# Optimization experiments

Measured on AMD Instinct MI355X. Metric: run time of the kernel, lower is better.

Reference implementation:

```python
import jax, jax.numpy as jnp
import numpy as np

B, K, S, HS = 32, 8, 512, 256


def setup_inputs() -> dict:
    key = jax.random.key(0)
    ks = jax.random.split(key, 12)
    sc = 1.0 / np.sqrt(HS)
    return {
        "rem_fea": jax.random.normal(ks[0], (B, S, HS), jnp.float32),
        "ret_fea": jax.random.normal(ks[1], (B, K, S, HS), jnp.float32),
        "Wr": jax.random.normal(ks[2], (HS, HS), jnp.float32) * sc,
        "br": jax.random.normal(ks[3], (HS,), jnp.float32) * sc,
        "Wt": jax.random.normal(ks[4], (HS, HS), jnp.float32) * sc,
        "bt": jax.random.normal(ks[5], (HS,), jnp.float32) * sc,
        "W1": jax.random.normal(ks[6], (K, HS, HS), jnp.float32) * sc,
        "b1": jax.random.normal(ks[7], (K, HS), jnp.float32) * sc,
        "W2": jax.random.normal(ks[8], (K, HS, HS), jnp.float32) * sc,
        "b2": jax.random.normal(ks[9], (K, HS), jnp.float32) * sc,
    }


def reference(rem_fea, ret_fea, Wr, br, Wt, bt, W1, b1, W2, b2):
    # ---- MACRouter ----
    rem_lin = rem_fea @ Wr + br                       # [B,S,hs]
    ret_lin = jnp.einsum("bksd,de->bkse", ret_fea, Wt) + bt  # [B,K,S,hs]
    avg_rem = rem_lin.mean(axis=1)                    # [B,hs]
    avg_ret = ret_lin.mean(axis=2)                    # [B,K,hs]
    scores = jnp.einsum("bd,bkd->bk", avg_rem, avg_ret)
    routing = jax.nn.softmax(scores, axis=1)          # [B,K]
    # ---- K dense experts (batched over K) ----
    h = jax.nn.relu(jnp.einsum("bksd,kde->bkse", ret_fea, W1) + b1[None, :, None, :])
    expert_outs = jnp.einsum("bksd,kde->bkse", h, W2) + b2[None, :, None, :]
    # ---- weighted sum over experts ----
    gen_fea = jnp.einsum("bksd,bk->bsd", expert_outs, routing)
    return gen_fea
```

## Files before the change

### kernel.cpp

```cpp
#include <hip/hip_runtime.h>
#include <hip/hip_bf16.h>

typedef __attribute__((ext_vector_type(8))) short bf16x8;
typedef __attribute__((ext_vector_type(4))) float f32x4;

constexpr int Bb = 32, Kk = 8, Ss = 512, HS = 256;
constexpr int SUB = 32;
constexpr int NST = Ss / SUB;
constexpr int SUB_BYTES = SUB * HS * 2;
constexpr int MT = 64;

__device__ __forceinline__ unsigned short f2bf(float f) {
  unsigned int u = __builtin_bit_cast(unsigned int, f);
  u = (u + 0x7FFFu + ((u >> 16) & 1u)) >> 16;
  return (unsigned short)u;
}

__device__ __forceinline__ void gload_lds16(const void* g, void* l) {
  __builtin_amdgcn_global_load_lds((const __attribute__((address_space(1))) void*)g,
                                   (__attribute__((address_space(3))) void*)l, 16, 0, 0);
}

__global__ void prep(const float* __restrict__ rem, const float* __restrict__ ret,
                     const float* __restrict__ W1, const float* __restrict__ W2,
                     unsigned short* __restrict__ W1p, unsigned short* __restrict__ W2p,
                     char* __restrict__ swz, float* __restrict__ partial_ret,
                     float* __restrict__ partial_rem) {
  int blk = blockIdx.x, t = threadIdx.x;
  if (blk < 512) {
    const float* W = (blk < 256) ? W1 : W2;
    unsigned short* Wp = (blk < 256) ? W1p : W2p;
    int idx = (blk & 255) * 256 + t;
    int lane = idx & 63, nt = (idx >> 6) & 15, kk = (idx >> 10) & 7, k = idx >> 13;
    const float* src = W + ((size_t)k * HS + kk * 32 + ((lane >> 4) * 8)) * HS + nt * 16 + (lane & 15);
    unsigned short* dst = Wp + (size_t)idx * 8;
#pragma unroll
    for (int i = 0; i < 8; ++i) dst[i] = f2bf(src[(size_t)i * HS]);
    return;
  }
  blk -= 512;
  const float* src;
  float* pdst;
  char* dst = nullptr;
  if (blk < Bb * Kk * NST) {
    int st = blk & 15, bk = blk >> 4;
    src = ret + ((size_t)bk * Ss + st * SUB) * HS;
    pdst = partial_ret + (size_t)blk * HS;
    if (swz) dst = swz + (size_t)blk * SUB_BYTES;
  } else {
    int rid = blk - Bb * Kk * NST;
    int st = rid & 15, b = rid >> 4;
    src = rem + ((size_t)b * Ss + st * SUB) * HS;
    pdst = partial_rem + (size_t)rid * HS;
  }
  f32x4 acc = {0.f, 0.f, 0.f, 0.f};
#pragma unroll
  for (int j = 0; j < 8; ++j) {
    int f = j * 256 + t;
    int row = f >> 6, c4 = f & 63;
    f32x4 v = *reinterpret_cast<const f32x4*>(src + (size_t)row * HS + c4 * 4);
    acc += v;
    if (dst) {
      union { unsigned short h[4]; unsigned long long u; } pk;
      pk.h[0] = f2bf(v[0]); pk.h[1] = f2bf(v[1]); pk.h[2] = f2bf(v[2]); pk.h[3] = f2bf(v[3]);
      int off = (c4 >> 5) * 8192 + row * 256 + ((((c4 & 31) >> 1) ^ (row & 7)) * 16) + (c4 & 1) * 8;
      *reinterpret_cast<unsigned long long*>(dst + off) = pk.u;
    }
  }
  __shared__ f32x4 red[256];
  red[t] = acc;
  __syncthreads();
  if (t < 64) {
    f32x4 s = red[t] + red[t + 64] + red[t + 128] + red[t + 192];
    *reinterpret_cast<f32x4*>(pdst + t * 4) = s;
  }
}

template <int SRC>
__launch_bounds__(512, 1)
__global__ void experts_kernel(const float* __restrict__ ret, const char* __restrict__ ret_swz,
                               const unsigned short* __restrict__ W1p,
                               const unsigned short* __restrict__ W2p,
                               const float* __restrict__ b1, const float* __restrict__ b2,
                               const float* __restrict__ partial_ret,
                               const float* __restrict__ partial_rem,
                               const float* __restrict__ Wr, const float* __restrict__ br,
                               const float* __restrict__ Wt, const float* __restrict__ bt,
                               float* __restrict__ out) {
  __shared__ __align__(16) char A_lds[2][2 * SUB_BYTES];
  __shared__ __align__(16) char H_lds[MT * HS * 2];
  __shared__ float srem_sh[HS];
  __shared__ float sret_sh[Kk][HS];
  __shared__ float shred[8];
  __shared__ float scores_sh[Kk];
  __shared__ float routing_sh[Kk];

  const int blk = blockIdx.x;
  const int b = blk >> 3, st64 = blk & 7;
  const int tid = threadIdx.x;
  const int wave = tid >> 6, lane = tid & 63;
  const int l15 = lane & 15, l4 = lane >> 4;
  const int t256 = tid & 255, half = tid >> 8;

  auto stage = [&](int k, int bufi) {
    if constexpr (SRC == 0) {
      const char* tb = ret_swz + ((size_t)((b * Kk + k) * NST + st64 * 2)) * SUB_BYTES;
#pragma unroll
      for (int i = 0; i < 4; ++i) {
        int c = wave + i * 8;
        gload_lds16(tb + c * 1024 + (size_t)lane * 16, A_lds[bufi] + c * 1024);
      }
    } else {
      const float* src = ret + ((size_t)(b * Kk + k) * Ss + st64 * MT) * HS;
#pragma unroll
      for (int j = 0; j < 8; ++j) {
        int f = j * 512 + tid;
        int row = f >> 6, c4 = f & 63;
        f32x4 v = *reinterpret_cast<const f32x4*>(src + (size_t)row * HS + c4 * 4);
        union { unsigned short h[4]; unsigned long long u; } pk;
        pk.h[0] = f2bf(v[0]); pk.h[1] = f2bf(v[1]); pk.h[2] = f2bf(v[2]); pk.h[3] = f2bf(v[3]);
        int off = (row >> 5) * 16384 + (c4 >> 5) * 8192 + (row & 31) * 256 +
                  ((((c4 & 31) >> 1) ^ (row & 7)) * 16) + (c4 & 1) * 8;
        *reinterpret_cast<unsigned long long*>(A_lds[bufi] + off) = pk.u;
      }
    }
  };

  stage(0, 0);

  {
#pragma unroll
    for (int kk = 0; kk < 4; ++kk) {
      int k = half * 4 + kk;
      float sk = 0.f;
      for (int st = 0; st < NST; ++st)
        sk += partial_ret[((size_t)((b * Kk + k) * NST + st)) * HS + t256];
      sret_sh[k][t256] = sk;
    }
    if (half == 1) {
      float s_ = 0.f;
      for (int st = 0; st < NST; ++st)
        s_ += partial_rem[((size_t)(b * NST + st)) * HS + t256];
      srem_sh[t256] = s_;
    }
    __syncthreads();

    float rl = 0.f;
    float tl[4] = {0.f, 0.f, 0.f, 0.f};
    for (int e = 0; e < HS; ++e) {
      float wr = Wr[(size_t)e * HS + t256];
      float wt = Wt[(size_t)e * HS + t256];
      rl += srem_sh[e] * wr;
#pragma unroll
      for (int kk = 0; kk < 4; ++kk) tl[kk] += sret_sh[half * 4 + kk][e] * wt;
    }
    rl = rl * (1.f / Ss) + br[t256];

    for (int kk = 0; kk < 4; ++kk) {
      float p = rl * (tl[kk] * (1.f / Ss) + bt[t256]);
#pragma unroll
      for (int off = 32; off; off >>= 1) p += __shfl_down(p, off);
      if (lane == 0) shred[wave] = p;
      __syncthreads();
      if (tid == 0) scores_sh[kk] = shred[0] + shred[1] + shred[2] + shred[3];
      else if (tid == 256) scores_sh[4 + kk] = shred[4] + shred[5] + shred[6] + shred[7];
      __syncthreads();
    }
    if (tid == 0) {
      float mx = scores_sh[0];
      for (int k = 1; k < Kk; ++k) mx = fmaxf(mx, scores_sh[k]);
      float ssum = 0.f, ev[Kk];
      for (int k = 0; k < Kk; ++k) { ev[k] = expf(scores_sh[k] - mx); ssum += ev[k]; }
      for (int k = 0; k < Kk; ++k) routing_sh[k] = ev[k] / ssum;
    }
  }
  asm volatile("s_waitcnt vmcnt(0) lgkmcnt(0)\n\ts_barrier" ::: "memory");

  f32x4 out_acc[4][2];
#pragma unroll
  for (int m = 0; m < 4; ++m)
#pragma unroll
    for (int n = 0; n < 2; ++n) out_acc[m][n] = {0.f, 0.f, 0.f, 0.f};
  const f32x4 zero4 = {0.f, 0.f, 0.f, 0.f};

  int buf = 0;
  for (int k = 0; k < Kk; ++k) {
    const unsigned short* W1k = W1p + (size_t)k * 65536;
    bf16x8 w1f[8][2];
#pragma unroll
    for (int kk = 0; kk < 8; ++kk)
#pragma unroll
      for (int m = 0; m < 2; ++m)
        w1f[kk][m] = *reinterpret_cast<const bf16x8*>(
            W1k + ((size_t)(kk * 16 + wave * 2 + m) * 64 + lane) * 8);

    if (k + 1 < Kk) stage(k + 1, buf ^ 1);

    f32x4 accH[2][4];
#pragma unroll
    for (int m = 0; m < 2; ++m)
#pragma unroll
      for (int n = 0; n < 4; ++n) accH[m][n] = zero4;

#pragma unroll
    for (int kk = 0; kk < 8; ++kk) {
      bf16x8 aA[4];
#pragma unroll
      for (int n = 0; n < 4; ++n) {
        int srow = n * 16 + l15;
        int r5 = srow & 31;
        int off = (srow >> 5) * 16384 + (kk >> 2) * 8192 + r5 * 256 +
                  ((((kk & 3) * 4 + l4) ^ (r5 & 7)) * 16);
        aA[n] = *reinterpret_cast<const bf16x8*>(A_lds[buf] + off);
      }
#pragma unroll
      for (int m = 0; m < 2; ++m)
#pragma unroll
        for (int n = 0; n < 4; ++n)
          accH[m][n] = __builtin_amdgcn_mfma_f32_16x16x32_bf16(w1f[kk][m], aA[n], accH[m][n], 0, 0, 0);
    }

    const unsigned short* W2k = W2p + (size_t)k * 65536;
    bf16x8 w2f[8][2];
#pragma unroll
    for (int kk = 0; kk < 8; ++kk)
#pragma unroll
      for (int n = 0; n < 2; ++n)
        w2f[kk][n] = *reinterpret_cast<const bf16x8*>(
            W2k + ((size_t)(kk * 16 + wave * 2 + n) * 64 + lane) * 8);

    {
      float r = routing_sh[k];
#pragma unroll
      for (int m = 0; m < 2; ++m) {
        int e0 = wave * 32 + m * 16 + l4 * 4;
        float4 b1v = *reinterpret_cast<const float4*>(b1 + k * HS + e0);
#pragma unroll
        for (int n = 0; n < 4; ++n) {
          int srow = n * 16 + l15;
          union { unsigned short h[4]; unsigned long long u; } pk;
          pk.h[0] = f2bf(fmaxf(accH[m][n][0] + b1v.x, 0.f) * r);
          pk.h[1] = f2bf(fmaxf(accH[m][n][1] + b1v.y, 0.f) * r);
          pk.h[2] = f2bf(fmaxf(accH[m][n][2] + b1v.z, 0.f) * r);
          pk.h[3] = f2bf(fmaxf(accH[m][n][3] + b1v.w, 0.f) * r);
          int boff = srow * 512 + ((e0 * 2) ^ ((srow & 7) << 4));
          *reinterpret_cast<unsigned long long*>(H_lds + boff) = pk.u;
        }
      }
    }

    asm volatile("s_waitcnt lgkmcnt(0)\n\ts_barrier" ::: "memory");

#pragma unroll
    for (int kk = 0; kk < 8; ++kk) {
      bf16x8 aH[4];
#pragma unroll
      for (int m = 0; m < 4; ++m) {
        int r = m * 16 + l15;
        int boff = r * 512 + ((kk * 64 + l4 * 16) ^ ((r & 7) << 4));
        aH[m] = *reinterpret_cast<const bf16x8*>(H_lds + boff);
      }
#pragma unroll
      for (int m = 0; m < 4; ++m)
#pragma unroll
        for (int n = 0; n < 2; ++n)
          out_acc[m][n] = __builtin_amdgcn_mfma_f32_16x16x32_bf16(aH[m], w2f[kk][n], out_acc[m][n], 0, 0, 0);
    }
    asm volatile("s_waitcnt vmcnt(0) lgkmcnt(0)\n\ts_barrier" ::: "memory");
    buf ^= 1;
  }

  float bias2[2];
#pragma unroll
  for (int n = 0; n < 2; ++n) {
    int col = (wave * 2 + n) * 16 + l15;
    float s = 0.f;
#pragma unroll
    for (int k = 0; k < Kk; ++k) s += routing_sh[k] * b2[k * HS + col];
    bias2[n] = s;
  }
#pragma unroll
  for (int m = 0; m < 4; ++m)
#pragma unroll
    for (int i = 0; i < 4; ++i) {
      int row = m * 16 + l4 * 4 + i;
      float* orow = out + ((size_t)b * Ss + st64 * MT + row) * HS;
#pragma unroll
      for (int n = 0; n < 2; ++n)
        orow[(wave * 2 + n) * 16 + l15] = out_acc[m][n][i] + bias2[n];
    }
}

extern "C" void kernel_launch(void* const* d_in, const int* in_sizes, int n_in,
                              void* d_out, int out_size, void* d_ws, size_t ws_size,
                              hipStream_t stream) {
  const float* rem = (const float*)d_in[0];
  const float* ret = (const float*)d_in[1];
  const float* Wr  = (const float*)d_in[2];
  const float* br  = (const float*)d_in[3];
  const float* Wt  = (const float*)d_in[4];
  const float* bt  = (const float*)d_in[5];
  const float* W1  = (const float*)d_in[6];
  const float* b1  = (const float*)d_in[7];
  const float* W2  = (const float*)d_in[8];
  const float* b2  = (const float*)d_in[9];
  float* out = (float*)d_out;

  char* w = (char*)d_ws;
  unsigned short* W1p = (unsigned short*)w;
  unsigned short* W2p = (unsigned short*)(w + (1u << 20));
  float* partial_ret  = (float*)(w + (2u << 20));
  float* partial_rem  = (float*)(w + (6u << 20));
  char*  ret_swz      = w + (7u << 20);

  bool full = ws_size >= ((size_t)71 << 20);

  prep<<<512 + Bb * Kk * NST + Bb * NST, 256, 0, stream>>>(rem, ret, W1, W2, W1p, W2p,
                                                           full ? ret_swz : nullptr,
                                                           partial_ret, partial_rem);
  if (full)
    experts_kernel<0><<<Bb * (Ss / MT), 512, 0, stream>>>(ret, ret_swz, W1p, W2p, b1, b2,
                                                          partial_ret, partial_rem,
                                                          Wr, br, Wt, bt, out);
  else
    experts_kernel<1><<<Bb * (Ss / MT), 512, 0, stream>>>(ret, nullptr, W1p, W2p, b1, b2,
                                                          partial_ret, partial_rem,
                                                          Wr, br, Wt, bt, out);
}
```

Baseline: 99.21 us.

## Drop pre-swizzled bf16 ret copy; register-prefetch fp32 tiles into LDS

Removes the prep-stage write of a swizzled bf16 copy of ret_fea and the experts kernel's direct global-to-LDS loads from it. The experts kernel now loads fp32 ret tiles into registers one expert ahead, then converts and writes them into the swizzled LDS buffer after the first GEMM's barrier. This avoids writing and re-reading a large intermediate buffer, at the cost of more registers per thread and more conversion work inside the main loop.

```diff
diff --git a/kernel.cpp b/kernel.cpp
--- a/kernel.cpp
+++ b/kernel.cpp
@@ -16,16 +16,10 @@
   return (unsigned short)u;
 }
 
-__device__ __forceinline__ void gload_lds16(const void* g, void* l) {
-  __builtin_amdgcn_global_load_lds((const __attribute__((address_space(1))) void*)g,
-                                   (__attribute__((address_space(3))) void*)l, 16, 0, 0);
-}
-
 __global__ void prep(const float* __restrict__ rem, const float* __restrict__ ret,
                      const float* __restrict__ W1, const float* __restrict__ W2,
                      unsigned short* __restrict__ W1p, unsigned short* __restrict__ W2p,
-                     char* __restrict__ swz, float* __restrict__ partial_ret,
-                     float* __restrict__ partial_rem) {
+                     float* __restrict__ partial_ret, float* __restrict__ partial_rem) {
   int blk = blockIdx.x, t = threadIdx.x;
   if (blk < 512) {
     const float* W = (blk < 256) ? W1 : W2;
@@ -41,12 +35,10 @@
   blk -= 512;
   const float* src;
   float* pdst;
-  char* dst = nullptr;
   if (blk < Bb * Kk * NST) {
     int st = blk & 15, bk = blk >> 4;
     src = ret + ((size_t)bk * Ss + st * SUB) * HS;
     pdst = partial_ret + (size_t)blk * HS;
-    if (swz) dst = swz + (size_t)blk * SUB_BYTES;
   } else {
     int rid = blk - Bb * Kk * NST;
     int st = rid & 15, b = rid >> 4;
@@ -57,15 +49,7 @@
 #pragma unroll
   for (int j = 0; j < 8; ++j) {
     int f = j * 256 + t;
-    int row = f >> 6, c4 = f & 63;
-    f32x4 v = *reinterpret_cast<const f32x4*>(src + (size_t)row * HS + c4 * 4);
-    acc += v;
-    if (dst) {
-      union { unsigned short h[4]; unsigned long long u; } pk;
-      pk.h[0] = f2bf(v[0]); pk.h[1] = f2bf(v[1]); pk.h[2] = f2bf(v[2]); pk.h[3] = f2bf(v[3]);
-      int off = (c4 >> 5) * 8192 + row * 256 + ((((c4 & 31) >> 1) ^ (row & 7)) * 16) + (c4 & 1) * 8;
-      *reinterpret_cast<unsigned long long*>(dst + off) = pk.u;
-    }
+    acc += *reinterpret_cast<const f32x4*>(src + (size_t)(f >> 6) * HS + (f & 63) * 4);
   }
   __shared__ f32x4 red[256];
   red[t] = acc;
@@ -76,9 +60,8 @@
   }
 }
 
-template <int SRC>
 __launch_bounds__(512, 1)
-__global__ void experts_kernel(const float* __restrict__ ret, const char* __restrict__ ret_swz,
+__global__ void experts_kernel(const float* __restrict__ ret,
                                const unsigned short* __restrict__ W1p,
                                const unsigned short* __restrict__ W2p,
                                const float* __restrict__ b1, const float* __restrict__ b2,
@@ -102,31 +85,32 @@
   const int l15 = lane & 15, l4 = lane >> 4;
   const int t256 = tid & 255, half = tid >> 8;
 
-  auto stage = [&](int k, int bufi) {
-    if constexpr (SRC == 0) {
-      const char* tb = ret_swz + ((size_t)((b * Kk + k) * NST + st64 * 2)) * SUB_BYTES;
-#pragma unroll
-      for (int i = 0; i < 4; ++i) {
-        int c = wave + i * 8;
-        gload_lds16(tb + c * 1024 + (size_t)lane * 16, A_lds[bufi] + c * 1024);
-      }
-    } else {
-      const float* src = ret + ((size_t)(b * Kk + k) * Ss + st64 * MT) * HS;
-#pragma unroll
-      for (int j = 0; j < 8; ++j) {
-        int f = j * 512 + tid;
-        int row = f >> 6, c4 = f & 63;
-        f32x4 v = *reinterpret_cast<const f32x4*>(src + (size_t)row * HS + c4 * 4);
-        union { unsigned short h[4]; unsigned long long u; } pk;
-        pk.h[0] = f2bf(v[0]); pk.h[1] = f2bf(v[1]); pk.h[2] = f2bf(v[2]); pk.h[3] = f2bf(v[3]);
-        int off = (row >> 5) * 16384 + (c4 >> 5) * 8192 + (row & 31) * 256 +
-                  ((((c4 & 31) >> 1) ^ (row & 7)) * 16) + (c4 & 1) * 8;
-        *reinterpret_cast<unsigned long long*>(A_lds[bufi] + off) = pk.u;
-      }
+  const float* tile0 = ret + ((size_t)(b * Kk) * Ss + st64 * MT) * HS;
+
+  auto stage_load = [&](int k, float4* ld) {
+    const float* src = tile0 + (size_t)k * Ss * HS;
+#pragma unroll
+    for (int j = 0; j < 8; ++j) {
+      int f = j * 512 + tid;
+      ld[j] = *reinterpret_cast<const float4*>(src + (size_t)(f >> 6) * HS + (f & 63) * 4);
     }
   };
-
-  stage(0, 0);
+  auto stage_write = [&](int bufi, const float4* ld) {
+#pragma unroll
+    for (int j = 0; j < 8; ++j) {
+      int f = j * 512 + tid;
+      int row = f >> 6, c4 = f & 63;
+      union { unsigned short h[4]; unsigned long long u; } pk;
+      pk.h[0] = f2bf(ld[j].x); pk.h[1] = f2bf(ld[j].y);
+      pk.h[2] = f2bf(ld[j].z); pk.h[3] = f2bf(ld[j].w);
+      int off = (row >> 5) * 16384 + (c4 >> 5) * 8192 + (row & 31) * 256 +
+                ((((c4 & 31) >> 1) ^ (row & 7)) * 16) + (c4 & 1) * 8;
+      *reinterpret_cast<unsigned long long*>(A_lds[bufi] + off) = pk.u;
+    }
+  };
+
+  float4 ld0[8];
+  stage_load(0, ld0);
 
   {
 #pragma unroll
@@ -174,6 +158,8 @@
       for (int k = 0; k < Kk; ++k) routing_sh[k] = ev[k] / ssum;
     }
   }
+  __syncthreads();
+  stage_write(0, ld0);
   asm volatile("s_waitcnt vmcnt(0) lgkmcnt(0)\n\ts_barrier" ::: "memory");
 
   f32x4 out_acc[4][2];
@@ -194,7 +180,8 @@
         w1f[kk][m] = *reinterpret_cast<const bf16x8*>(
             W1k + ((size_t)(kk * 16 + wave * 2 + m) * 64 + lane) * 8);
 
-    if (k + 1 < Kk) stage(k + 1, buf ^ 1);
+    float4 ld[8];
+    if (k + 1 < Kk) stage_load(k + 1, ld);
 
     f32x4 accH[2][4];
 #pragma unroll
@@ -250,6 +237,8 @@
     }
 
     asm volatile("s_waitcnt lgkmcnt(0)\n\ts_barrier" ::: "memory");
+
+    if (k + 1 < Kk) stage_write(buf ^ 1, ld);
 
 #pragma unroll
     for (int kk = 0; kk < 8; ++kk) {
@@ -311,19 +300,10 @@
   unsigned short* W2p = (unsigned short*)(w + (1u << 20));
   float* partial_ret  = (float*)(w + (2u << 20));
   float* partial_rem  = (float*)(w + (6u << 20));
-  char*  ret_swz      = w + (7u << 20);
-
-  bool full = ws_size >= ((size_t)71 << 20);
 
   prep<<<512 + Bb * Kk * NST + Bb * NST, 256, 0, stream>>>(rem, ret, W1, W2, W1p, W2p,
-                                                           full ? ret_swz : nullptr,
                                                            partial_ret, partial_rem);
-  if (full)
-    experts_kernel<0><<<Bb * (Ss / MT), 512, 0, stream>>>(ret, ret_swz, W1p, W2p, b1, b2,
-                                                          partial_ret, partial_rem,
-                                                          Wr, br, Wt, bt, out);
-  else
-    experts_kernel<1><<<Bb * (Ss / MT), 512, 0, stream>>>(ret, nullptr, W1p, W2p, b1, b2,
-                                                          partial_ret, partial_rem,
-                                                          Wr, br, Wt, bt, out);
+  experts_kernel<<<Bb * (Ss / MT), 512, 0, stream>>>(ret, W1p, W2p, b1, b2,
+                                                     partial_ret, partial_rem,
+                                                     Wr, br, Wt, bt, out);
 }
```

New measurement: 124.7 us. +25.7%, slower.
